# Optimization experiments

Hardware: AMD Instinct MI355X
Metric: run time of the kernel (lower is better)

The kernel has to match this reference:

```python
import jax, jax.numpy as jnp
import numpy as np

DIM = 256
DIM_HEAD = 32
HEADS = DIM // DIM_HEAD
WSZ = 8
SCALE = DIM_HEAD ** -0.5
DPB_DIM = DIM // 4  # 64
EPS = 1e-5

# precomputed integer relative-position index table [wsz^2, wsz^2]
_pos = np.arange(WSZ)
_gi, _gj = np.meshgrid(_pos, _pos, indexing='ij')
_grid = np.stack([_gi, _gj], -1).reshape(WSZ * WSZ, 2)
_rel = _grid[:, None] - _grid[None, :]
_rel[..., 0] += WSZ - 1
_rel[..., 1] += WSZ - 1
REL_POS_IDX = jnp.asarray(_rel[..., 0] * (2 * WSZ - 1) + _rel[..., 1])  # [64,64], max 224

# continuous relative coords fed to the DPB MLP: (2*wsz+1)^2 = 289 points
_p = np.arange(-WSZ, WSZ + 1)
_ri, _rj = np.meshgrid(_p, _p, indexing='ij')
REL_COORDS = jnp.asarray(np.stack([_ri, _rj], -1).reshape(-1, 2).astype(np.float32))  # [289,2]


def _ln(h, gamma, beta):
    mu = h.mean(axis=-1, keepdims=True)
    var = jnp.var(h, axis=-1, keepdims=True)
    return (h - mu) / jnp.sqrt(var + EPS) * gamma + beta


def _channel_ln(x, g, b):
    # channel-first (BCHW) layer norm, unbiased=False variance
    mu = x.mean(axis=1, keepdims=True)
    var = jnp.var(x, axis=1, keepdims=True)
    return (x - mu) / jnp.sqrt(var + EPS) * g[None, :, None, None] + b[None, :, None, None]


def _dpb(w1, b1, g1, be1, w2, b2, g2, be2, w3, b3, g3, be3, w4, b4):
    h = jax.nn.relu(_ln(REL_COORDS @ w1.T + b1, g1, be1))
    h = jax.nn.relu(_ln(h @ w2.T + b2, g2, be2))
    h = jax.nn.relu(_ln(h @ w3.T + b3, g3, be3))
    return (h @ w4.T + b4)[:, 0]  # [289]


def _forward(x, g, b, w_qkv, w_out, b_out,
             dpb_w1, dpb_b1, dpb_g1, dpb_be1,
             dpb_w2, dpb_b2, dpb_g2, dpb_be2,
             dpb_w3, dpb_b3, dpb_g3, dpb_be3,
             dpb_w4, dpb_b4):
    B, D, H, W = x.shape
    nh, nw = H // WSZ, W // WSZ
    n = WSZ * WSZ

    xn = _channel_ln(x, g, b)
    # short-range windows: b d (h s1) (w s2) -> (b h w) d (s1 s2)
    xw = xn.reshape(B, D, nh, WSZ, nw, WSZ).transpose(0, 2, 4, 1, 3, 5).reshape(B * nh * nw, D, n)

    qkv = jnp.einsum('od,bdn->bon', w_qkv, xw)  # [nB, 3*D, n]
    q, k, v = jnp.split(qkv, 3, axis=1)
    def heads(t):  # [nB, D, n] -> [nB, h, n, dh]
        return t.reshape(-1, HEADS, DIM_HEAD, n).transpose(0, 1, 3, 2)
    q, k, v = heads(q), heads(k), heads(v)

    sim = jnp.einsum('bhid,bhjd->bhij', q * SCALE, k)  # [nB, h, n, n]
    dpb_vals = _dpb(dpb_w1, dpb_b1, dpb_g1, dpb_be1,
                    dpb_w2, dpb_b2, dpb_g2, dpb_be2,
                    dpb_w3, dpb_b3, dpb_g3, dpb_be3,
                    dpb_w4, dpb_b4)
    bias = dpb_vals[REL_POS_IDX]  # [n, n]
    attn = jax.nn.softmax(sim + bias, axis=-1)
    out = jnp.einsum('bhij,bhjd->bhid', attn, v)  # [nB, h, n, dh]
    out = out.transpose(0, 1, 3, 2).reshape(-1, D, n)  # [nB, D, n]
    out = jnp.einsum('od,bdn->bon', w_out, out) + b_out[None, :, None]
    # back to (B, D, H, W)
    out = out.reshape(B, nh, nw, D, WSZ, WSZ).transpose(0, 3, 1, 4, 2, 5).reshape(B, D, H, W)
    return out


def setup_inputs() -> dict:
    key = jax.random.key(0)
    ks = jax.random.split(key, 12)
    s = 0.05
    d = DPB_DIM
    inp = {
        'x': jax.random.normal(ks[0], (2, 256, 256, 256), jnp.float32),
        'g': jnp.ones((DIM,), jnp.float32),
        'b': jnp.zeros((DIM,), jnp.float32),
        'w_qkv': jax.random.normal(ks[1], (3 * DIM, DIM), jnp.float32) * s,
        'w_out': jax.random.normal(ks[2], (DIM, DIM), jnp.float32) * s,
        'b_out': jnp.zeros((DIM,), jnp.float32),
        'dpb_w1': jax.random.normal(ks[3], (d, 2), jnp.float32) * s,
        'dpb_b1': jnp.zeros((d,), jnp.float32),
        'dpb_g1': jnp.ones((d,), jnp.float32),
        'dpb_be1': jnp.zeros((d,), jnp.float32),
        'dpb_w2': jax.random.normal(ks[4], (d, d), jnp.float32) * s,
        'dpb_b2': jnp.zeros((d,), jnp.float32),
        'dpb_g2': jnp.ones((d,), jnp.float32),
        'dpb_be2': jnp.zeros((d,), jnp.float32),
        'dpb_w3': jax.random.normal(ks[5], (d, d), jnp.float32) * s,
        'dpb_b3': jnp.zeros((d,), jnp.float32),
        'dpb_g3': jnp.ones((d,), jnp.float32),
        'dpb_be3': jnp.zeros((d,), jnp.float32),
        'dpb_w4': jax.random.normal(ks[6], (1, d), jnp.float32) * s,
        'dpb_b4': jnp.zeros((1,), jnp.float32),
    }
    return inp


def reference(x, g, b, w_qkv, w_out, b_out,
              dpb_w1, dpb_b1, dpb_g1, dpb_be1,
              dpb_w2, dpb_b2, dpb_g2, dpb_be2,
              dpb_w3, dpb_b3, dpb_g3, dpb_be3,
              dpb_w4, dpb_b4):
    return _forward(x, g, b, w_qkv, w_out, b_out,
                    dpb_w1, dpb_b1, dpb_g1, dpb_be1,
                    dpb_w2, dpb_b2, dpb_g2, dpb_be2,
                    dpb_w3, dpb_b3, dpb_g3, dpb_be3,
                    dpb_w4, dpb_b4)
```

## Files before the change

### kernel.cpp

```cpp
#include <hip/hip_runtime.h>

typedef __attribute__((ext_vector_type(8))) short short8;
typedef __attribute__((ext_vector_type(4))) float f32x4;
typedef unsigned short ushort_t;
typedef unsigned int uint_t;

#define MFMA16(a, b, c) __builtin_amdgcn_mfma_f32_16x16x32_bf16((a), (b), (c), 0, 0, 0)

__device__ __forceinline__ ushort_t f2bf(float f) {
    union { float f; uint_t u; } c; c.f = f;
    uint_t u = c.u;
    uint_t r = (u + 0x7FFFu + ((u >> 16) & 1u)) >> 16;
    return (ushort_t)r;
}
__device__ __forceinline__ uint_t pack2(float a, float b) {
    return (uint_t)f2bf(a) | ((uint_t)f2bf(b) << 16);
}

__device__ __forceinline__ float wredsum(float v) {
    #pragma unroll
    for (int m = 1; m < 64; m <<= 1) v += __shfl_xor(v, m);
    return v;
}

__global__ void dpb_vals_kernel(const float* __restrict__ w1, const float* __restrict__ b1,
                                const float* __restrict__ g1, const float* __restrict__ be1,
                                const float* __restrict__ w2, const float* __restrict__ b2,
                                const float* __restrict__ g2, const float* __restrict__ be2,
                                const float* __restrict__ w3, const float* __restrict__ b3,
                                const float* __restrict__ g3, const float* __restrict__ be3,
                                const float* __restrict__ w4, const float* __restrict__ b4,
                                float* __restrict__ valsg) {
    int wv = threadIdx.x >> 6, j = threadIdx.x & 63;
    int pt = blockIdx.x * 8 + wv;
    if (pt >= 289) return;
    float ri = (float)(pt / 17 - 8), rj = (float)(pt % 17 - 8);

    float t = ri * w1[2 * j] + rj * w1[2 * j + 1] + b1[j];
    float mu = wredsum(t) * (1.f / 64.f);
    float d = t - mu;
    float var = wredsum(d * d) * (1.f / 64.f);
    float h = fmaxf(0.f, d * rsqrtf(var + 1e-5f) * g1[j] + be1[j]);

    float a = b2[j];
    for (int k = 0; k < 64; ++k) a += __shfl(h, k) * w2[j * 64 + k];
    mu = wredsum(a) * (1.f / 64.f);
    d = a - mu;
    var = wredsum(d * d) * (1.f / 64.f);
    h = fmaxf(0.f, d * rsqrtf(var + 1e-5f) * g2[j] + be2[j]);

    a = b3[j];
    for (int k = 0; k < 64; ++k) a += __shfl(h, k) * w3[j * 64 + k];
    mu = wredsum(a) * (1.f / 64.f);
    d = a - mu;
    var = wredsum(d * d) * (1.f / 64.f);
    h = fmaxf(0.f, d * rsqrtf(var + 1e-5f) * g3[j] + be3[j]);

    float v = wredsum(h * w4[j]) + b4[0];
    if (j == 0) valsg[pt] = v;
}

__global__ void cvt_kernel(const float* __restrict__ wqkv, const float* __restrict__ wout,
                           const float* __restrict__ valsg,
                           ushort_t* __restrict__ wbf, float* __restrict__ biasg) {
    int i = blockIdx.x * 512 + threadIdx.x;
    if (i < 196608) {
        wbf[i] = f2bf(wqkv[i]);
    } else if (i < 262144) {
        wbf[i] = f2bf(wout[i - 196608]);
    } else {
        int idx = i - 262144;
        int r = idx >> 6, c = idx & 63;
        int p = ((r >> 3) - (c >> 3) + 7) * 15 + ((r & 7) - (c & 7) + 7);
        biasg[idx] = valsg[p];
    }
}

#define LDS_BYTES 156160
#define SCALE_Q 0.17677669529663687f

__global__ __launch_bounds__(512) void win_attn(
    const float* __restrict__ x, const float* __restrict__ gamw, const float* __restrict__ betw,
    const ushort_t* __restrict__ wqkv, const ushort_t* __restrict__ wout,
    const float* __restrict__ boutp, const float* __restrict__ biasg,
    float* __restrict__ outp) {
    extern __shared__ char smem[];
    const int tid = threadIdx.x;
    const int wid = blockIdx.x;
    const int bb = wid >> 10, rem = wid & 1023, wh = rem >> 5, ww = rem & 31;
    const int xoff = bb * 16777216 + wh * 2048 + ww * 8;
    const float* xb = x + xoff;

    float* Xs = (float*)smem;
    char* XNb = smem + 118784;
    float* red = (float*)(smem + 151552);
    float* muv = (float*)(smem + 155648);

    #pragma unroll
    for (int it = 0; it < 8; ++it) {
        int idx = it * 512 + tid;
        int d = idx >> 4, p4 = idx & 15;
        int py = p4 >> 1, c4 = (p4 & 1) << 2;
        float4 v = *(const float4*)(xb + d * 65536 + py * 256 + c4);
        *(float4*)&Xs[d * 64 + py * 8 + c4] = v;
    }
    __syncthreads();

    {
        int n = tid & 63, dq = tid >> 6;
        float s = 0.f, s2 = 0.f;
        #pragma unroll
        for (int i2 = 0; i2 < 32; ++i2) {
            float v = Xs[(dq * 32 + i2) * 64 + n];
            s += v; s2 += v * v;
        }
        red[dq * 64 + n] = s;
        red[512 + dq * 64 + n] = s2;
    }
    __syncthreads();
    if (tid < 64) {
        float s = 0.f, s2 = 0.f;
        #pragma unroll
        for (int q = 0; q < 8; ++q) { s += red[q * 64 + tid]; s2 += red[512 + q * 64 + tid]; }
        float mu = s * 0.00390625f;
        float var = s2 * 0.00390625f - mu * mu;
        muv[tid] = mu;
        muv[64 + tid] = rsqrtf(var + 1e-5f);
    }
    __syncthreads();

    {
        int n = tid & 63, dc = tid >> 6;
        float mu = muv[n], rs = muv[64 + n];
        #pragma unroll
        for (int jj = 0; jj < 4; ++jj) {
            int d0 = dc * 32 + jj * 8;
            uint_t p0, p1, p2, p3;
            {
                float a0 = (Xs[(d0 + 0) * 64 + n] - mu) * rs * gamw[d0 + 0] + betw[d0 + 0];
                float a1 = (Xs[(d0 + 1) * 64 + n] - mu) * rs * gamw[d0 + 1] + betw[d0 + 1];
                float a2 = (Xs[(d0 + 2) * 64 + n] - mu) * rs * gamw[d0 + 2] + betw[d0 + 2];
                float a3 = (Xs[(d0 + 3) * 64 + n] - mu) * rs * gamw[d0 + 3] + betw[d0 + 3];
                float a4 = (Xs[(d0 + 4) * 64 + n] - mu) * rs * gamw[d0 + 4] + betw[d0 + 4];
                float a5 = (Xs[(d0 + 5) * 64 + n] - mu) * rs * gamw[d0 + 5] + betw[d0 + 5];
                float a6 = (Xs[(d0 + 6) * 64 + n] - mu) * rs * gamw[d0 + 6] + betw[d0 + 6];
                float a7 = (Xs[(d0 + 7) * 64 + n] - mu) * rs * gamw[d0 + 7] + betw[d0 + 7];
                p0 = pack2(a0, a1); p1 = pack2(a2, a3); p2 = pack2(a4, a5); p3 = pack2(a6, a7);
            }
            int bo = (n << 9) + (d0 << 1);
            bo ^= ((bo >> 9) & 7) << 4;
            uint4 q4; q4.x = p0; q4.y = p1; q4.z = p2; q4.w = p3;
            *(uint4*)(XNb + bo) = q4;
        }
    }
    __syncthreads();

    const int wv = tid >> 6, l = tid & 63, g = l >> 4, m15 = l & 15;

    {
        f32x4 acc[6][4] = {};
        for (int kt = 0; kt < 8; ++kt) {
            short8 bfr[4];
            #pragma unroll
            for (int nt = 0; nt < 4; ++nt) {
                int bo = ((nt * 16 + m15) << 9) + kt * 64 + g * 16;
                bo ^= ((bo >> 9) & 7) << 4;
                bfr[nt] = *(const short8*)(XNb + bo);
            }
            #pragma unroll
            for (int mt = 0; mt < 6; ++mt) {
                int row = wv * 96 + mt * 16 + m15;
                short8 afr = *(const short8*)(wqkv + row * 256 + kt * 32 + g * 8);
                #pragma unroll
                for (int nt = 0; nt < 4; ++nt)
                    acc[mt][nt] = MFMA16(afr, bfr[nt], acc[mt][nt]);
            }
        }
        #pragma unroll
        for (int mt = 0; mt < 6; ++mt) {
            int rowb = wv * 96 + mt * 16 + g * 4;
            int sec = rowb >> 8;
            int h = (rowb >> 5) & 7;
            int dh = rowb & 31;
            char* base = smem + h * 14848 + (sec == 2 ? 10240 : sec * 5120);
            #pragma unroll
            for (int nt = 0; nt < 4; ++nt) {
                f32x4 a = acc[mt][nt];
                if (sec == 0) { a[0] *= SCALE_Q; a[1] *= SCALE_Q; a[2] *= SCALE_Q; a[3] *= SCALE_Q; }
                int n = nt * 16 + m15;
                if (sec < 2) {
                    uint2 pv; pv.x = pack2(a[0], a[1]); pv.y = pack2(a[2], a[3]);
                    *(uint2*)(base + n * 80 + dh * 2) = pv;
                } else {
                    #pragma unroll
                    for (int e = 0; e < 4; ++e)
                        *(ushort_t*)(base + (dh + e) * 144 + n * 2) = f2bf(a[e]);
                }
            }
        }
    }
    __syncthreads();

    {
        char* Qb = smem + wv * 14848;
        char* Kb = Qb + 5120;
        char* Vb = Qb + 10240;
        char* Pb = Qb;

        short8 qa[4], kf[4];
        #pragma unroll
        for (int t4 = 0; t4 < 4; ++t4) {
            qa[t4] = *(const short8*)(Qb + (t4 * 16 + m15) * 80 + g * 16);
            kf[t4] = *(const short8*)(Kb + (t4 * 16 + m15) * 80 + g * 16);
        }
        f32x4 s[4][4];
        #pragma unroll
        for (int mt = 0; mt < 4; ++mt)
            #pragma unroll
            for (int nt = 0; nt < 4; ++nt) {
                f32x4 z = {};
                s[mt][nt] = MFMA16(qa[mt], kf[nt], z);
            }
        #pragma unroll
        for (int mt = 0; mt < 4; ++mt) {
            #pragma unroll
            for (int e = 0; e < 4; ++e) {
                int i = mt * 16 + g * 4 + e;
                const float* brow = biasg + i * 64 + m15;
                s[mt][0][e] += brow[0];
                s[mt][1][e] += brow[16];
                s[mt][2][e] += brow[32];
                s[mt][3][e] += brow[48];
                float mx = fmaxf(fmaxf(s[mt][0][e], s[mt][1][e]), fmaxf(s[mt][2][e], s[mt][3][e]));
                for (int xm = 1; xm < 16; xm <<= 1) mx = fmaxf(mx, __shfl_xor(mx, xm));
                float sum = 0.f;
                #pragma unroll
                for (int nt = 0; nt < 4; ++nt) {
                    float p = __expf(s[mt][nt][e] - mx);
                    s[mt][nt][e] = p; sum += p;
                }
                for (int xm = 1; xm < 16; xm <<= 1) sum += __shfl_xor(sum, xm);
                float inv = 1.f / sum;
                #pragma unroll
                for (int nt = 0; nt < 4; ++nt) s[mt][nt][e] *= inv;
            }
        }
        #pragma unroll
        for (int mt = 0; mt < 4; ++mt)
            #pragma unroll
            for (int nt = 0; nt < 4; ++nt)
                #pragma unroll
                for (int e = 0; e < 4; ++e) {
                    int i = mt * 16 + g * 4 + e, j = nt * 16 + m15;
                    *(ushort_t*)(Pb + i * 144 + j * 2) = f2bf(s[mt][nt][e]);
                }
        f32x4 o2[2][4] = {};
        #pragma unroll
        for (int ks = 0; ks < 2; ++ks) {
            short8 pb[4];
            #pragma unroll
            for (int nt = 0; nt < 4; ++nt)
                pb[nt] = *(const short8*)(Pb + (nt * 16 + m15) * 144 + ks * 64 + g * 16);
            #pragma unroll
            for (int mt2 = 0; mt2 < 2; ++mt2) {
                short8 va = *(const short8*)(Vb + (mt2 * 16 + m15) * 144 + ks * 64 + g * 16);
                #pragma unroll
                for (int nt = 0; nt < 4; ++nt)
                    o2[mt2][nt] = MFMA16(va, pb[nt], o2[mt2][nt]);
            }
        }
        #pragma unroll
        for (int mt2 = 0; mt2 < 2; ++mt2)
            #pragma unroll
            for (int nt = 0; nt < 4; ++nt) {
                int i = nt * 16 + m15;
                int dd = wv * 32 + mt2 * 16 + g * 4;
                int bo = (i << 9) + (dd << 1);
                bo ^= ((bo >> 9) & 7) << 4;
                uint2 pv;
                pv.x = pack2(o2[mt2][nt][0], o2[mt2][nt][1]);
                pv.y = pack2(o2[mt2][nt][2], o2[mt2][nt][3]);
                *(uint2*)(XNb + bo) = pv;
            }
    }
    __syncthreads();

    {
        f32x4 po[2][4] = {};
        for (int kt = 0; kt < 8; ++kt) {
            short8 bfr[4];
            #pragma unroll
            for (int nt = 0; nt < 4; ++nt) {
                int bo = ((nt * 16 + m15) << 9) + kt * 64 + g * 16;
                bo ^= ((bo >> 9) & 7) << 4;
                bfr[nt] = *(const short8*)(XNb + bo);
            }
            #pragma unroll
            for (int mt = 0; mt < 2; ++mt) {
                int row = wv * 32 + mt * 16 + m15;
                short8 afr = *(const short8*)(wout + row * 256 + kt * 32 + g * 8);
                #pragma unroll
                for (int nt = 0; nt < 4; ++nt)
                    po[mt][nt] = MFMA16(afr, bfr[nt], po[mt][nt]);
            }
        }
        float* ob = outp + xoff;
        #pragma unroll
        for (int mt = 0; mt < 2; ++mt) {
            int o0 = wv * 32 + mt * 16 + g * 4;
            float bo0 = boutp[o0], bo1 = boutp[o0 + 1], bo2 = boutp[o0 + 2], bo3 = boutp[o0 + 3];
            #pragma unroll
            for (int nt = 0; nt < 4; ++nt) {
                int i = nt * 16 + m15;
                int pix = (i >> 3) * 256 + (i & 7);
                ob[(o0 + 0) * 65536 + pix] = po[mt][nt][0] + bo0;
                ob[(o0 + 1) * 65536 + pix] = po[mt][nt][1] + bo1;
                ob[(o0 + 2) * 65536 + pix] = po[mt][nt][2] + bo2;
                ob[(o0 + 3) * 65536 + pix] = po[mt][nt][3] + bo3;
            }
        }
    }
}

extern "C" void kernel_launch(void* const* d_in, const int* in_sizes, int n_in,
                              void* d_out, int out_size, void* d_ws, size_t ws_size,
                              hipStream_t stream) {
    const float* x     = (const float*)d_in[0];
    const float* g     = (const float*)d_in[1];
    const float* b     = (const float*)d_in[2];
    const float* w_qkv = (const float*)d_in[3];
    const float* w_out = (const float*)d_in[4];
    const float* b_out = (const float*)d_in[5];
    const float* dw1 = (const float*)d_in[6],  *db1 = (const float*)d_in[7];
    const float* dg1 = (const float*)d_in[8],  *dbe1 = (const float*)d_in[9];
    const float* dw2 = (const float*)d_in[10], *db2 = (const float*)d_in[11];
    const float* dg2 = (const float*)d_in[12], *dbe2 = (const float*)d_in[13];
    const float* dw3 = (const float*)d_in[14], *db3 = (const float*)d_in[15];
    const float* dg3 = (const float*)d_in[16], *dbe3 = (const float*)d_in[17];
    const float* dw4 = (const float*)d_in[18], *db4 = (const float*)d_in[19];

    ushort_t* wbf   = (ushort_t*)d_ws;
    float*    biasg = (float*)((char*)d_ws + 524288);
    float*    valsg = (float*)((char*)d_ws + 540672);

    hipLaunchKernelGGL(dpb_vals_kernel, dim3(37), dim3(512), 0, stream,
                       dw1, db1, dg1, dbe1, dw2, db2, dg2, dbe2,
                       dw3, db3, dg3, dbe3, dw4, db4, valsg);
    hipLaunchKernelGGL(cvt_kernel, dim3(520), dim3(512), 0, stream,
                       w_qkv, w_out, valsg, wbf, biasg);

    (void)hipFuncSetAttribute((const void*)win_attn,
                              hipFuncAttributeMaxDynamicSharedMemorySize, LDS_BYTES);
    hipLaunchKernelGGL(win_attn, dim3(2048), dim3(512), LDS_BYTES, stream,
                       x, g, b, wbf, wbf + 196608, b_out, biasg, (float*)d_out);
}
```

Baseline: 554.7 us.

## Shrink LDS footprint, keep Q and P in registers, reorder QKV weights

Stores the input window tile in LDS as bf16 instead of fp32, which cuts LDS from about 152KB to about 69KB so more blocks can be resident per CU. The QKV weight rows are permuted and the Q rows pre-scaled, so each wave's accumulators hold exactly its own head's Q, K and V. Q and the softmax probabilities are rearranged with cross-lane shuffles instead of being written to LDS, and the bias table is pre-laid-out to match the register fragment order. Block indices are also swizzled across batches. This risks higher register pressure and rounds x to bf16 before the LayerNorm statistics are computed, which loses precision.

```diff
diff --git a/kernel.cpp b/kernel.cpp
--- a/kernel.cpp
+++ b/kernel.cpp
@@ -6,6 +6,7 @@
 typedef unsigned int uint_t;
 
 #define MFMA16(a, b, c) __builtin_amdgcn_mfma_f32_16x16x32_bf16((a), (b), (c), 0, 0, 0)
+#define SCALE_Q 0.17677669529663687f
 
 __device__ __forceinline__ ushort_t f2bf(float f) {
     union { float f; uint_t u; } c; c.f = f;
@@ -15,6 +16,9 @@
 }
 __device__ __forceinline__ uint_t pack2(float a, float b) {
     return (uint_t)f2bf(a) | ((uint_t)f2bf(b) << 16);
+}
+__device__ __forceinline__ float bf2f(ushort_t u) {
+    union { float f; uint_t x; } c; c.x = ((uint_t)u) << 16; return c.f;
 }
 
 __device__ __forceinline__ float wredsum(float v) {
@@ -62,39 +66,49 @@
 
 __global__ void cvt_kernel(const float* __restrict__ wqkv, const float* __restrict__ wout,
                            const float* __restrict__ valsg,
-                           ushort_t* __restrict__ wbf, float* __restrict__ biasg) {
+                           ushort_t* __restrict__ wbf, float* __restrict__ biasR) {
     int i = blockIdx.x * 512 + threadIdx.x;
     if (i < 196608) {
-        wbf[i] = f2bf(wqkv[i]);
+        int r = i >> 8, c = i & 255;
+        int wv = r / 96, s = r % 96;
+        int src = (s < 32) ? (wv * 32 + s) : (s < 64) ? (256 + wv * 32 + s - 32)
+                                                      : (512 + wv * 32 + s - 64);
+        float f = wqkv[src * 256 + c];
+        if (s < 32) f *= SCALE_Q;
+        wbf[i] = f2bf(f);
     } else if (i < 262144) {
         wbf[i] = f2bf(wout[i - 196608]);
     } else {
         int idx = i - 262144;
-        int r = idx >> 6, c = idx & 63;
-        int p = ((r >> 3) - (c >> 3) + 7) * 15 + ((r & 7) - (c & 7) + 7);
-        biasg[idx] = valsg[p];
-    }
-}
-
-#define LDS_BYTES 156160
-#define SCALE_Q 0.17677669529663687f
-
-__global__ __launch_bounds__(512) void win_attn(
+        int l = idx >> 6, r6 = idx & 63;
+        int nts = r6 >> 4, mts = (r6 >> 2) & 3, e = r6 & 3;
+        int ii = nts * 16 + (l & 15);
+        int jj = mts * 16 + ((l >> 4) << 2) + e;
+        int p = ((ii >> 3) - (jj >> 3) + 7) * 15 + ((ii & 7) - (jj & 7) + 7);
+        biasR[idx] = valsg[p];
+    }
+}
+
+#define LDS_BYTES 70144
+
+__global__ __launch_bounds__(512, 4) void win_attn(
     const float* __restrict__ x, const float* __restrict__ gamw, const float* __restrict__ betw,
     const ushort_t* __restrict__ wqkv, const ushort_t* __restrict__ wout,
-    const float* __restrict__ boutp, const float* __restrict__ biasg,
+    const float* __restrict__ boutp, const float* __restrict__ biasR,
     float* __restrict__ outp) {
     extern __shared__ char smem[];
     const int tid = threadIdx.x;
-    const int wid = blockIdx.x;
+    const int wid = ((blockIdx.x & 7) << 8) | (blockIdx.x >> 3);
     const int bb = wid >> 10, rem = wid & 1023, wh = rem >> 5, ww = rem & 31;
     const int xoff = bb * 16777216 + wh * 2048 + ww * 8;
     const float* xb = x + xoff;
 
-    float* Xs = (float*)smem;
-    char* XNb = smem + 118784;
-    float* red = (float*)(smem + 151552);
-    float* muv = (float*)(smem + 155648);
+    char* Xs  = smem;
+    char* XNb = smem + 32768;
+    float* red = (float*)(smem + 65536);
+    float* muv = (float*)(smem + 69632);
+
+    const int wv = tid >> 6, l = tid & 63, g = l >> 4, m15 = l & 15;
 
     #pragma unroll
     for (int it = 0; it < 8; ++it) {
@@ -102,16 +116,19 @@
         int d = idx >> 4, p4 = idx & 15;
         int py = p4 >> 1, c4 = (p4 & 1) << 2;
         float4 v = *(const float4*)(xb + d * 65536 + py * 256 + c4);
-        *(float4*)&Xs[d * 64 + py * 8 + c4] = v;
+        uint2 w; w.x = pack2(v.x, v.y); w.y = pack2(v.z, v.w);
+        int bo = (d * 128 + (py * 8 + c4) * 2) ^ ((d & 7) << 4);
+        *(uint2*)(Xs + bo) = w;
     }
     __syncthreads();
 
     {
-        int n = tid & 63, dq = tid >> 6;
+        int n = l, dq = wv;
         float s = 0.f, s2 = 0.f;
         #pragma unroll
         for (int i2 = 0; i2 < 32; ++i2) {
-            float v = Xs[(dq * 32 + i2) * 64 + n];
+            int d = dq * 32 + i2;
+            float v = bf2f(*(const ushort_t*)(Xs + ((d * 128 + n * 2) ^ ((d & 7) << 4))));
             s += v; s2 += v * v;
         }
         red[dq * 64 + n] = s;
@@ -130,35 +147,192 @@
     __syncthreads();
 
     {
-        int n = tid & 63, dc = tid >> 6;
+        int n = l, dc = wv;
         float mu = muv[n], rs = muv[64 + n];
         #pragma unroll
         for (int jj = 0; jj < 4; ++jj) {
             int d0 = dc * 32 + jj * 8;
-            uint_t p0, p1, p2, p3;
-            {
-                float a0 = (Xs[(d0 + 0) * 64 + n] - mu) * rs * gamw[d0 + 0] + betw[d0 + 0];
-                float a1 = (Xs[(d0 + 1) * 64 + n] - mu) * rs * gamw[d0 + 1] + betw[d0 + 1];
-                float a2 = (Xs[(d0 + 2) * 64 + n] - mu) * rs * gamw[d0 + 2] + betw[d0 + 2];
-                float a3 = (Xs[(d0 + 3) * 64 + n] - mu) * rs * gamw[d0 + 3] + betw[d0 + 3];
-                float a4 = (Xs[(d0 + 4) * 64 + n] - mu) * rs * gamw[d0 + 4] + betw[d0 + 4];
-                float a5 = (Xs[(d0 + 5) * 64 + n] - mu) * rs * gamw[d0 + 5] + betw[d0 + 5];
-                float a6 = (Xs[(d0 + 6) * 64 + n] - mu) * rs * gamw[d0 + 6] + betw[d0 + 6];
-                float a7 = (Xs[(d0 + 7) * 64 + n] - mu) * rs * gamw[d0 + 7] + betw[d0 + 7];
-                p0 = pack2(a0, a1); p1 = pack2(a2, a3); p2 = pack2(a4, a5); p3 = pack2(a6, a7);
-            }
-            int bo = (n << 9) + (d0 << 1);
+            uint_t p[4];
+            #pragma unroll
+            for (int h = 0; h < 4; ++h) {
+                int da = d0 + 2 * h, db = d0 + 2 * h + 1;
+                float va = bf2f(*(const ushort_t*)(Xs + ((da * 128 + n * 2) ^ ((da & 7) << 4))));
+                float vb = bf2f(*(const ushort_t*)(Xs + ((db * 128 + n * 2) ^ ((db & 7) << 4))));
+                float aa = (va - mu) * rs * gamw[da] + betw[da];
+                float ab = (vb - mu) * rs * gamw[db] + betw[db];
+                p[h] = pack2(aa, ab);
+            }
+            int bo = ((n << 9) + (d0 << 1));
             bo ^= ((bo >> 9) & 7) << 4;
-            uint4 q4; q4.x = p0; q4.y = p1; q4.z = p2; q4.w = p3;
+            uint4 q4; q4.x = p[0]; q4.y = p[1]; q4.z = p[2]; q4.w = p[3];
             *(uint4*)(XNb + bo) = q4;
         }
     }
     __syncthreads();
 
-    const int wv = tid >> 6, l = tid & 63, g = l >> 4, m15 = l & 15;
-
+    f32x4 acc[6][4] = {};
+    for (int kt = 0; kt < 8; ++kt) {
+        short8 bfr[4];
+        #pragma unroll
+        for (int nt = 0; nt < 4; ++nt) {
+            int bo = ((nt * 16 + m15) << 9) + kt * 64 + g * 16;
+            bo ^= ((bo >> 9) & 7) << 4;
+            bfr[nt] = *(const short8*)(XNb + bo);
+        }
+        #pragma unroll
+        for (int mt = 0; mt < 6; ++mt) {
+            short8 afr = *(const short8*)(wqkv + (wv * 96 + mt * 16 + m15) * 256 + kt * 32 + g * 8);
+            #pragma unroll
+            for (int nt = 0; nt < 4; ++nt)
+                acc[mt][nt] = MFMA16(afr, bfr[nt], acc[mt][nt]);
+        }
+    }
+    __syncthreads();
+
+    char* Ksh = XNb + wv * 4096;
+    char* Vsh = Xs  + wv * 4096;
+
+    #pragma unroll
+    for (int mtk = 0; mtk < 2; ++mtk)
+        #pragma unroll
+        for (int nt = 0; nt < 4; ++nt) {
+            int j = nt * 16 + m15;
+            uint2 w; w.x = pack2(acc[2 + mtk][nt][0], acc[2 + mtk][nt][1]);
+                     w.y = pack2(acc[2 + mtk][nt][2], acc[2 + mtk][nt][3]);
+            *(uint2*)(Ksh + j * 64 + (mtk * 16 + g * 4) * 2) = w;
+        }
+    #pragma unroll
+    for (int mtv = 0; mtv < 2; ++mtv)
+        #pragma unroll
+        for (int nt = 0; nt < 4; ++nt)
+            #pragma unroll
+            for (int e = 0; e < 4; ++e) {
+                int d = mtv * 16 + g * 4 + e;
+                int bo = (d * 128 + (nt * 16 + m15) * 2) ^ ((d & 7) << 4);
+                *(ushort_t*)(Vsh + bo) = f2bf(acc[4 + mtv][nt][e]);
+            }
+
+    const int srcA = (((2 * g) & 3) << 4) | m15;
+    const int srcB = (((2 * g + 1) & 3) << 4) | m15;
+    const bool hi = (g >= 2);
+    union F8 { short8 v; uint_t u[4]; };
+    F8 qf[4];
+    #pragma unroll
+    for (int t = 0; t < 4; ++t) {
+        uint_t a0 = pack2(acc[0][t][0], acc[0][t][1]);
+        uint_t a1 = pack2(acc[0][t][2], acc[0][t][3]);
+        uint_t b0 = pack2(acc[1][t][0], acc[1][t][1]);
+        uint_t b1 = pack2(acc[1][t][2], acc[1][t][3]);
+        uint_t wA0 = __shfl(a0, srcA), wA1 = __shfl(a1, srcA);
+        uint_t wB0 = __shfl(a0, srcB), wB1 = __shfl(a1, srcB);
+        uint_t xA0 = __shfl(b0, srcA), xA1 = __shfl(b1, srcA);
+        uint_t xB0 = __shfl(b0, srcB), xB1 = __shfl(b1, srcB);
+        qf[t].u[0] = hi ? xA0 : wA0;
+        qf[t].u[1] = hi ? xA1 : wA1;
+        qf[t].u[2] = hi ? xB0 : wB0;
+        qf[t].u[3] = hi ? xB1 : wB1;
+    }
+
+    f32x4 s[4][4];
     {
-        f32x4 acc[6][4] = {};
+        short8 kfr[4];
+        #pragma unroll
+        for (int mts = 0; mts < 4; ++mts)
+            kfr[mts] = *(const short8*)(Ksh + (mts * 16 + m15) * 64 + g * 16);
+        #pragma unroll
+        for (int mts = 0; mts < 4; ++mts)
+            #pragma unroll
+            for (int nts = 0; nts < 4; ++nts) {
+                f32x4 z = {};
+                s[mts][nts] = MFMA16(kfr[mts], qf[nts].v, z);
+            }
+    }
+
+    #pragma unroll
+    for (int nts = 0; nts < 4; ++nts) {
+        const float* brp = biasR + l * 64 + nts * 16;
+        float4 br0 = *(const float4*)(brp);
+        float4 br1 = *(const float4*)(brp + 4);
+        float4 br2 = *(const float4*)(brp + 8);
+        float4 br3 = *(const float4*)(brp + 12);
+        s[0][nts][0] += br0.x; s[0][nts][1] += br0.y; s[0][nts][2] += br0.z; s[0][nts][3] += br0.w;
+        s[1][nts][0] += br1.x; s[1][nts][1] += br1.y; s[1][nts][2] += br1.z; s[1][nts][3] += br1.w;
+        s[2][nts][0] += br2.x; s[2][nts][1] += br2.y; s[2][nts][2] += br2.z; s[2][nts][3] += br2.w;
+        s[3][nts][0] += br3.x; s[3][nts][1] += br3.y; s[3][nts][2] += br3.z; s[3][nts][3] += br3.w;
+
+        float mx = s[0][nts][0];
+        #pragma unroll
+        for (int mts = 0; mts < 4; ++mts)
+            #pragma unroll
+            for (int e = 0; e < 4; ++e) mx = fmaxf(mx, s[mts][nts][e]);
+        mx = fmaxf(mx, __shfl_xor(mx, 16));
+        mx = fmaxf(mx, __shfl_xor(mx, 32));
+        float sum = 0.f;
+        #pragma unroll
+        for (int mts = 0; mts < 4; ++mts)
+            #pragma unroll
+            for (int e = 0; e < 4; ++e) {
+                float p = __expf(s[mts][nts][e] - mx);
+                s[mts][nts][e] = p; sum += p;
+            }
+        sum += __shfl_xor(sum, 16);
+        sum += __shfl_xor(sum, 32);
+        float inv = 1.f / sum;
+        #pragma unroll
+        for (int mts = 0; mts < 4; ++mts)
+            #pragma unroll
+            for (int e = 0; e < 4; ++e) s[mts][nts][e] *= inv;
+    }
+
+    f32x4 o2[2][4] = {};
+    #pragma unroll
+    for (int ks = 0; ks < 2; ++ks) {
+        F8 pb[4];
+        #pragma unroll
+        for (int t = 0; t < 4; ++t) {
+            uint_t a0 = pack2(s[ks * 2 + 0][t][0], s[ks * 2 + 0][t][1]);
+            uint_t a1 = pack2(s[ks * 2 + 0][t][2], s[ks * 2 + 0][t][3]);
+            uint_t b0 = pack2(s[ks * 2 + 1][t][0], s[ks * 2 + 1][t][1]);
+            uint_t b1 = pack2(s[ks * 2 + 1][t][2], s[ks * 2 + 1][t][3]);
+            uint_t wA0 = __shfl(a0, srcA), wA1 = __shfl(a1, srcA);
+            uint_t wB0 = __shfl(a0, srcB), wB1 = __shfl(a1, srcB);
+            uint_t xA0 = __shfl(b0, srcA), xA1 = __shfl(b1, srcA);
+            uint_t xB0 = __shfl(b0, srcB), xB1 = __shfl(b1, srcB);
+            pb[t].u[0] = hi ? xA0 : wA0;
+            pb[t].u[1] = hi ? xA1 : wA1;
+            pb[t].u[2] = hi ? xB0 : wB0;
+            pb[t].u[3] = hi ? xB1 : wB1;
+        }
+        #pragma unroll
+        for (int mt2 = 0; mt2 < 2; ++mt2) {
+            int d = mt2 * 16 + m15;
+            int vo = (d * 128 + ks * 64 + g * 16) ^ ((d & 7) << 4);
+            short8 va = *(const short8*)(Vsh + vo);
+            #pragma unroll
+            for (int t = 0; t < 4; ++t)
+                o2[mt2][t] = MFMA16(va, pb[t].v, o2[mt2][t]);
+        }
+    }
+
+    __syncthreads();
+
+    #pragma unroll
+    for (int mt2 = 0; mt2 < 2; ++mt2)
+        #pragma unroll
+        for (int t = 0; t < 4; ++t) {
+            int i = t * 16 + m15;
+            int dd = wv * 32 + mt2 * 16 + g * 4;
+            int bo = (i << 9) + (dd << 1);
+            bo ^= ((bo >> 9) & 7) << 4;
+            uint2 pv;
+            pv.x = pack2(o2[mt2][t][0], o2[mt2][t][1]);
+            pv.y = pack2(o2[mt2][t][2], o2[mt2][t][3]);
+            *(uint2*)(XNb + bo) = pv;
+        }
+    __syncthreads();
+
+    {
+        f32x4 po[2][4] = {};
         for (int kt = 0; kt < 8; ++kt) {
             short8 bfr[4];
             #pragma unroll
@@ -168,137 +342,8 @@
                 bfr[nt] = *(const short8*)(XNb + bo);
             }
             #pragma unroll
-            for (int mt = 0; mt < 6; ++mt) {
-                int row = wv * 96 + mt * 16 + m15;
-                short8 afr = *(const short8*)(wqkv + row * 256 + kt * 32 + g * 8);
-                #pragma unroll
-                for (int nt = 0; nt < 4; ++nt)
-                    acc[mt][nt] = MFMA16(afr, bfr[nt], acc[mt][nt]);
-            }
-        }
-        #pragma unroll
-        for (int mt = 0; mt < 6; ++mt) {
-            int rowb = wv * 96 + mt * 16 + g * 4;
-            int sec = rowb >> 8;
-            int h = (rowb >> 5) & 7;
-            int dh = rowb & 31;
-            char* base = smem + h * 14848 + (sec == 2 ? 10240 : sec * 5120);
-            #pragma unroll
-            for (int nt = 0; nt < 4; ++nt) {
-                f32x4 a = acc[mt][nt];
-                if (sec == 0) { a[0] *= SCALE_Q; a[1] *= SCALE_Q; a[2] *= SCALE_Q; a[3] *= SCALE_Q; }
-                int n = nt * 16 + m15;
-                if (sec < 2) {
-                    uint2 pv; pv.x = pack2(a[0], a[1]); pv.y = pack2(a[2], a[3]);
-                    *(uint2*)(base + n * 80 + dh * 2) = pv;
-                } else {
-                    #pragma unroll
-                    for (int e = 0; e < 4; ++e)
-                        *(ushort_t*)(base + (dh + e) * 144 + n * 2) = f2bf(a[e]);
-                }
-            }
-        }
-    }
-    __syncthreads();
-
-    {
-        char* Qb = smem + wv * 14848;
-        char* Kb = Qb + 5120;
-        char* Vb = Qb + 10240;
-        char* Pb = Qb;
-
-        short8 qa[4], kf[4];
-        #pragma unroll
-        for (int t4 = 0; t4 < 4; ++t4) {
-            qa[t4] = *(const short8*)(Qb + (t4 * 16 + m15) * 80 + g * 16);
-            kf[t4] = *(const short8*)(Kb + (t4 * 16 + m15) * 80 + g * 16);
-        }
-        f32x4 s[4][4];
-        #pragma unroll
-        for (int mt = 0; mt < 4; ++mt)
-            #pragma unroll
-            for (int nt = 0; nt < 4; ++nt) {
-                f32x4 z = {};
-                s[mt][nt] = MFMA16(qa[mt], kf[nt], z);
-            }
-        #pragma unroll
-        for (int mt = 0; mt < 4; ++mt) {
-            #pragma unroll
-            for (int e = 0; e < 4; ++e) {
-                int i = mt * 16 + g * 4 + e;
-                const float* brow = biasg + i * 64 + m15;
-                s[mt][0][e] += brow[0];
-                s[mt][1][e] += brow[16];
-                s[mt][2][e] += brow[32];
-                s[mt][3][e] += brow[48];
-                float mx = fmaxf(fmaxf(s[mt][0][e], s[mt][1][e]), fmaxf(s[mt][2][e], s[mt][3][e]));
-                for (int xm = 1; xm < 16; xm <<= 1) mx = fmaxf(mx, __shfl_xor(mx, xm));
-                float sum = 0.f;
-                #pragma unroll
-                for (int nt = 0; nt < 4; ++nt) {
-                    float p = __expf(s[mt][nt][e] - mx);
-                    s[mt][nt][e] = p; sum += p;
-                }
-                for (int xm = 1; xm < 16; xm <<= 1) sum += __shfl_xor(sum, xm);
-                float inv = 1.f / sum;
-                #pragma unroll
-                for (int nt = 0; nt < 4; ++nt) s[mt][nt][e] *= inv;
-            }
-        }
-        #pragma unroll
-        for (int mt = 0; mt < 4; ++mt)
-            #pragma unroll
-            for (int nt = 0; nt < 4; ++nt)
-                #pragma unroll
-                for (int e = 0; e < 4; ++e) {
-                    int i = mt * 16 + g * 4 + e, j = nt * 16 + m15;
-                    *(ushort_t*)(Pb + i * 144 + j * 2) = f2bf(s[mt][nt][e]);
-                }
-        f32x4 o2[2][4] = {};
-        #pragma unroll
-        for (int ks = 0; ks < 2; ++ks) {
-            short8 pb[4];
-            #pragma unroll
-            for (int nt = 0; nt < 4; ++nt)
-                pb[nt] = *(const short8*)(Pb + (nt * 16 + m15) * 144 + ks * 64 + g * 16);
-            #pragma unroll
-            for (int mt2 = 0; mt2 < 2; ++mt2) {
-                short8 va = *(const short8*)(Vb + (mt2 * 16 + m15) * 144 + ks * 64 + g * 16);
-                #pragma unroll
-                for (int nt = 0; nt < 4; ++nt)
-                    o2[mt2][nt] = MFMA16(va, pb[nt], o2[mt2][nt]);
-            }
-        }
-        #pragma unroll
-        for (int mt2 = 0; mt2 < 2; ++mt2)
-            #pragma unroll
-            for (int nt = 0; nt < 4; ++nt) {
-                int i = nt * 16 + m15;
-                int dd = wv * 32 + mt2 * 16 + g * 4;
-                int bo = (i << 9) + (dd << 1);
-                bo ^= ((bo >> 9) & 7) << 4;
-                uint2 pv;
-                pv.x = pack2(o2[mt2][nt][0], o2[mt2][nt][1]);
-                pv.y = pack2(o2[mt2][nt][2], o2[mt2][nt][3]);
-                *(uint2*)(XNb + bo) = pv;
-            }
-    }
-    __syncthreads();
-
-    {
-        f32x4 po[2][4] = {};
-        for (int kt = 0; kt < 8; ++kt) {
-            short8 bfr[4];
-            #pragma unroll
-            for (int nt = 0; nt < 4; ++nt) {
-                int bo = ((nt * 16 + m15) << 9) + kt * 64 + g * 16;
-                bo ^= ((bo >> 9) & 7) << 4;
-                bfr[nt] = *(const short8*)(XNb + bo);
-            }
-            #pragma unroll
             for (int mt = 0; mt < 2; ++mt) {
-                int row = wv * 32 + mt * 16 + m15;
-                short8 afr = *(const short8*)(wout + row * 256 + kt * 32 + g * 8);
+                short8 afr = *(const short8*)(wout + (wv * 32 + mt * 16 + m15) * 256 + kt * 32 + g * 8);
                 #pragma unroll
                 for (int nt = 0; nt < 4; ++nt)
                     po[mt][nt] = MFMA16(afr, bfr[nt], po[mt][nt]);
@@ -340,17 +385,17 @@
     const float* dw4 = (const float*)d_in[18], *db4 = (const float*)d_in[19];
 
     ushort_t* wbf   = (ushort_t*)d_ws;
-    float*    biasg = (float*)((char*)d_ws + 524288);
+    float*    biasR = (float*)((char*)d_ws + 524288);
     float*    valsg = (float*)((char*)d_ws + 540672);
 
     hipLaunchKernelGGL(dpb_vals_kernel, dim3(37), dim3(512), 0, stream,
                        dw1, db1, dg1, dbe1, dw2, db2, dg2, dbe2,
                        dw3, db3, dg3, dbe3, dw4, db4, valsg);
     hipLaunchKernelGGL(cvt_kernel, dim3(520), dim3(512), 0, stream,
-                       w_qkv, w_out, valsg, wbf, biasg);
+                       w_qkv, w_out, valsg, wbf, biasR);
 
     (void)hipFuncSetAttribute((const void*)win_attn,
                               hipFuncAttributeMaxDynamicSharedMemorySize, LDS_BYTES);
     hipLaunchKernelGGL(win_attn, dim3(2048), dim3(512), LDS_BYTES, stream,
-                       x, g, b, wbf, wbf + 196608, b_out, biasg, (float*)d_out);
-}
+                       x, g, b, wbf, wbf + 196608, b_out, biasR, (float*)d_out);
+}
```

Result: slower. 778.4 us (+40.3%).
